# Optimization experiments

Hardware: AMD Instinct MI355X
Metric: run time of the kernel (lower is better)

Reference implementation:

```python
import jax, jax.numpy as jnp
import numpy as np
from jax import lax

C = 512   # n_feat == Cn == Cdim (forced by DA_conv/CA_layer consistency)
H, W = 16, 32  # reshape_codebooks(512)
K = 3     # kernel_size
RED = 8   # reduction


def _lrelu(x):
    return jax.nn.leaky_relu(x, 0.1)


def _conv1x1(x, w, b=None):
    # x: (B,C,H,W), w: (O,C) -- torch Conv2d(.,.,1) weight squeezed
    y = jnp.einsum('oc,bchw->bohw', w, x)
    if b is not None:
        y = y + b[None, :, None, None]
    return y


def _conv3x3(x, w, b):
    # x: (B,C,H,W), w: (O,C,3,3) OIHW, padding=k//2 == SAME for odd k
    y = lax.conv_general_dilated(x, w, (1, 1), 'SAME',
                                 dimension_numbers=('NCHW', 'OIHW', 'NCHW'))
    return y + b[None, :, None, None]


def _da_conv(c, deg, kw1, kw2, pw, pb, caw1, caw2):
    # per-channel dynamic kernels from degradation vectors: (Cn, K*K)
    kern = (_lrelu(deg @ kw1.T) @ kw2.T).reshape(C, 1, K, K)
    # depthwise conv, groups = b1*c1 = C (b1 == 1)
    out = lax.conv_general_dilated(c, kern, (1, 1), 'SAME',
                                   feature_group_count=C,
                                   dimension_numbers=('NCHW', 'OIHW', 'NCHW'))
    out = _lrelu(out)
    out = _conv1x1(out, pw, pb)
    # CA_layer: deg reshaped to (1, Cn, 16, 32), channel attention, deg * att
    dr = deg.reshape(1, C, H, W)
    att = jax.nn.sigmoid(_conv1x1(_lrelu(_conv1x1(dr, caw1)), caw2))
    return out + dr * att


def setup_inputs() -> dict:
    key = jax.random.key(0)
    ks = jax.random.split(key, 16)
    n = lambda i, shape, s=0.05: jax.random.normal(ks[i], shape, dtype=jnp.float32) * s
    return dict(
        c=jax.random.normal(ks[0], (1, C, H, W), dtype=jnp.float32),
        deg=jax.random.normal(ks[1], (C, C), dtype=jnp.float32) * 0.1,
        k1_w1=n(2, (C, C)), k1_w2=n(3, (K * K, C)),
        p1_w=n(4, (C, C)), p1_b=jnp.zeros((C,), jnp.float32),
        ca1_w1=n(5, (C // RED, C)), ca1_w2=n(6, (C, C // RED)),
        conv1_w=n(7, (C, C, K, K)), conv1_b=jnp.zeros((C,), jnp.float32),
        k2_w1=n(8, (C, C)), k2_w2=n(9, (K * K, C)),
        p2_w=n(10, (C, C)), p2_b=jnp.zeros((C,), jnp.float32),
        ca2_w1=n(11, (C // RED, C)), ca2_w2=n(12, (C, C // RED)),
        conv2_w=n(13, (C, C, K, K)), conv2_b=jnp.zeros((C,), jnp.float32),
    )


def reference(c, deg, k1_w1, k1_w2, p1_w, p1_b, ca1_w1, ca1_w2,
              conv1_w, conv1_b, k2_w1, k2_w2, p2_w, p2_b,
              ca2_w1, ca2_w2, conv2_w, conv2_b):
    out = _lrelu(_da_conv(c, deg, k1_w1, k1_w2, p1_w, p1_b, ca1_w1, ca1_w2))
    out = _lrelu(_conv3x3(out, conv1_w, conv1_b))
    out = _lrelu(_da_conv(out, deg, k2_w1, k2_w2, p2_w, p2_b, ca2_w1, ca2_w2))
    return _conv3x3(out, conv2_w, conv2_b) + c
```

## Files before the change

kernel.cpp:

```cpp
#include <hip/hip_runtime.h>
#include <hip/hip_bf16.h>

typedef __attribute__((ext_vector_type(8))) unsigned short ushort8;
typedef __attribute__((ext_vector_type(8))) __bf16 bf16x8;
typedef __attribute__((ext_vector_type(4))) float f32x4;
typedef __attribute__((ext_vector_type(4))) unsigned short ushort4v;

__device__ __forceinline__ float lrelu_f(float v){ return v > 0.f ? v : 0.1f*v; }

__device__ __forceinline__ unsigned short f2bf(float v){
  unsigned u = __float_as_uint(v);
  unsigned r = (u + 0x7fffu + ((u>>16)&1u)) >> 16;
  return (unsigned short)r;
}
__device__ __forceinline__ float bf2f(unsigned short u){
  return __uint_as_float(((unsigned)u)<<16);
}

__device__ __forceinline__ void gload16(const void* g, void* l){
  __builtin_amdgcn_global_load_lds(
    (const __attribute__((address_space(1))) unsigned int*)g,
    (__attribute__((address_space(3))) unsigned int*)l, 16, 0, 0);
}

__device__ __forceinline__ void packq(const float* __restrict__ s,
                                      unsigned short* __restrict__ d, int i){
  const float4 v = ((const float4*)s)[i];
  ushort4v o; o.x=f2bf(v.x); o.y=f2bf(v.y); o.z=f2bf(v.z); o.w=f2bf(v.w);
  *(ushort4v*)(d + (size_t)i*4) = o;
}

__global__ __launch_bounds__(256) void k_pack_all(
  const float* __restrict__ k1_w1, const float* __restrict__ k2_w1,
  const float* __restrict__ p1_w,  const float* __restrict__ p2_w,
  const float* __restrict__ ca1_w1,const float* __restrict__ ca1_w2,
  const float* __restrict__ ca2_w1,const float* __restrict__ ca2_w2,
  const float* __restrict__ deg,
  unsigned short* __restrict__ K1B, unsigned short* __restrict__ K2B,
  unsigned short* __restrict__ P1B, unsigned short* __restrict__ P2B,
  unsigned short* __restrict__ CA1A,unsigned short* __restrict__ CA1B,
  unsigned short* __restrict__ CA2A,unsigned short* __restrict__ CA2B,
  unsigned short* __restrict__ DEGB,unsigned short* __restrict__ DEGT){
  int i = blockIdx.x*256 + threadIdx.x;
  if (i < 65536){ packq(k1_w1, K1B, i); return; } i -= 65536;
  if (i < 65536){ packq(k2_w1, K2B, i); return; } i -= 65536;
  if (i < 65536){ packq(p1_w,  P1B, i); return; } i -= 65536;
  if (i < 65536){ packq(p2_w,  P2B, i); return; } i -= 65536;
  if (i < 8192){ packq(ca1_w1, CA1A, i); return; } i -= 8192;
  if (i < 8192){ packq(ca1_w2, CA1B, i); return; } i -= 8192;
  if (i < 8192){ packq(ca2_w1, CA2A, i); return; } i -= 8192;
  if (i < 8192){ packq(ca2_w2, CA2B, i); return; } i -= 8192;
  if (i < 65536){ packq(deg, DEGB, i); return; } i -= 65536;
  if (i < 65536){
    const int j = i*4; const int p = j>>9, c = j&511;
    ushort4v o;
    o.x = f2bf(deg[(size_t)(c+0)*512 + p]);
    o.y = f2bf(deg[(size_t)(c+1)*512 + p]);
    o.z = f2bf(deg[(size_t)(c+2)*512 + p]);
    o.w = f2bf(deg[(size_t)(c+3)*512 + p]);
    *(ushort4v*)(DEGT + (size_t)j) = o;
  }
}

__device__ __forceinline__ void gemm32(
    const unsigned short* __restrict__ A, const unsigned short* __restrict__ Bt,
    int m0, int n0, int K, int tid,
    unsigned short* lA, unsigned short* lB, f32x4& acc){
  const int wid = tid>>6, lane = tid&63;
  const int half = tid>>7, st_ = tid&127;
  const int srow = st_>>2, skb = st_&3;
  const unsigned short* gS = (half ? Bt + (size_t)(n0+srow)*K
                                   : A  + (size_t)(m0+srow)*K);
  unsigned short* lS = half ? lB : lA;
  const int soff0 = srow*64 + 8*(skb ^ (srow&7));
  const int soff1 = srow*64 + 8*((skb+4) ^ (srow&7));

  const int wr = (wid>>1)*16, wc = (wid&1)*16;
  const int l15 = lane&15, lkb = lane>>4;
  int aoff[2], boff[2];
  #pragma unroll
  for (int h=0;h<2;h++){
    const int Ra = wr + l15;
    aoff[h] = Ra*64 + 8*((lkb+4*h) ^ (Ra&7));
    const int Rb = wc + l15;
    boff[h] = Rb*64 + 8*((lkb+4*h) ^ (Rb&7));
  }

  const int nst = K>>6;
  ushort8 r0 = *(const ushort8*)(gS + skb*8);
  ushort8 r1 = *(const ushort8*)(gS + (skb+4)*8);
  *(ushort8*)(lS + soff0) = r0;
  *(ushort8*)(lS + soff1) = r1;
  if (nst > 1){
    r0 = *(const ushort8*)(gS + 64 + skb*8);
    r1 = *(const ushort8*)(gS + 64 + (skb+4)*8);
  }
  __syncthreads();
  for (int st=0; st<nst; ++st){
    const int cur = (st&1)*2048;
    bf16x8 af[2], bf[2];
    #pragma unroll
    for (int h=0;h<2;h++){
      af[h] = *(const bf16x8*)(lA + cur + aoff[h]);
      bf[h] = *(const bf16x8*)(lB + cur + boff[h]);
    }
    if (st+1 < nst){
      const int nxt = ((st+1)&1)*2048;
      *(ushort8*)(lS + nxt + soff0) = r0;
      *(ushort8*)(lS + nxt + soff1) = r1;
      if (st+2 < nst){
        r0 = *(const ushort8*)(gS + (size_t)(st+2)*64 + skb*8);
        r1 = *(const ushort8*)(gS + (size_t)(st+2)*64 + (skb+4)*8);
      }
    }
    #pragma unroll
    for (int h=0;h<2;h++)
      acc = __builtin_amdgcn_mfma_f32_16x16x32_bf16(af[h], bf[h], acc, 0,0,0);
    __syncthreads();
  }
}

__global__ __launch_bounds__(256) void k_mgemm_pre(
    const unsigned short* __restrict__ DEGB, const unsigned short* __restrict__ DEGT,
    const unsigned short* __restrict__ K1B,  const unsigned short* __restrict__ K2B,
    const unsigned short* __restrict__ CA1A, const unsigned short* __restrict__ CA2A,
    const float* __restrict__ conv1_w, const float* __restrict__ conv2_w,
    float* __restrict__ TMP1, float* __restrict__ TMP2,
    unsigned short* __restrict__ HID1, unsigned short* __restrict__ HID2,
    unsigned short* __restrict__ WB1, unsigned short* __restrict__ WB2){
  const int z = blockIdx.z;
  if (z >= 2 && blockIdx.y >= 2){
    const float* src      = (z==2) ? conv1_w : conv2_w;
    unsigned short* dst   = (z==2) ? WB1 : WB2;
    const int base = (((blockIdx.y-2)*16 + blockIdx.x)*256) + threadIdx.x;
    for (int i = base; i < 589824; i += 57344){
      const int o_ = i/1152; const int r4 = (i - o_*1152)*4;
      const int t = r4>>9; const int ci = r4&511;
      const float* s = src + (size_t)o_*4608;
      ushort4v o;
      o.x = f2bf(s[(ci+0)*9 + t]); o.y = f2bf(s[(ci+1)*9 + t]);
      o.z = f2bf(s[(ci+2)*9 + t]); o.w = f2bf(s[(ci+3)*9 + t]);
      *(ushort4v*)(dst + (size_t)o_*4608 + r4) = o;
    }
    return;
  }
  const unsigned short* A  = (z < 2) ? DEGB : DEGT;
  const unsigned short* Bt = (z==0) ? K1B : (z==1) ? K2B : (z==2) ? CA1A : CA2A;
  __shared__ unsigned short lA[4096], lB[4096];
  const int tid = threadIdx.x;
  const int m0 = blockIdx.x*32, n0 = blockIdx.y*32;
  f32x4 acc = {};
  gemm32(A, Bt, m0, n0, 512, tid, lA, lB, acc);

  const int wid = tid>>6, lane = tid&63;
  const int wr = (wid>>1)*16, wc = (wid&1)*16;
  const int l15 = lane&15, lkb = lane>>4;
  #pragma unroll
  for (int r=0;r<4;r++){
    const int row = m0 + wr + lkb*4 + r;
    const int col = n0 + wc + l15;
    const float v = lrelu_f(acc[r]);
    if (z==0)      TMP1[(size_t)row*512 + col] = v;
    else if (z==1) TMP2[(size_t)row*512 + col] = v;
    else if (z==2) HID1[(size_t)row*64 + col] = f2bf(v);
    else           HID2[(size_t)row*64 + col] = f2bf(v);
  }
}

__device__ __forceinline__ void gemm64(
    const unsigned short* __restrict__ A, const unsigned short* __restrict__ Bt,
    int m0, int n0, int K, int tid,
    unsigned short* lA, unsigned short* lB, f32x4 acc[2][2]){
  const int wid = tid>>6, lane = tid&63;
  const int srow = tid>>2, skb = tid&3;
  const unsigned short* gA = A  + (size_t)(m0+srow)*K + skb*8;
  const unsigned short* gB = Bt + (size_t)(n0+srow)*K + skb*8;
  const int soff = srow*32 + 8*(skb ^ (srow&3));
  const int wr = (wid>>1)*32, wc = (wid&1)*32;
  const int l15 = lane&15, lkb = lane>>4;
  int aoff[2], boff[2];
  #pragma unroll
  for (int s=0;s<2;s++){
    const int Ra = wr + s*16 + l15;
    aoff[s] = Ra*32 + 8*(lkb ^ (Ra&3));
    const int Rb = wc + s*16 + l15;
    boff[s] = Rb*32 + 8*(lkb ^ (Rb&3));
  }
  const int nst = K>>5;
  ushort8 ra = *(const ushort8*)gA;
  ushort8 rb = *(const ushort8*)gB;
  *(ushort8*)(lA + soff) = ra;
  *(ushort8*)(lB + soff) = rb;
  if (nst > 1){ ra = *(const ushort8*)(gA+32); rb = *(const ushort8*)(gB+32); }
  __syncthreads();
  for (int st=0; st<nst; ++st){
    const int cur = (st&1)*2048;
    bf16x8 af[2], bfr[2];
    #pragma unroll
    for (int s=0;s<2;s++){
      af[s]  = *(const bf16x8*)(lA + cur + aoff[s]);
      bfr[s] = *(const bf16x8*)(lB + cur + boff[s]);
    }
    if (st+1 < nst){
      const int nxt = ((st+1)&1)*2048;
      *(ushort8*)(lA + nxt + soff) = ra;
      *(ushort8*)(lB + nxt + soff) = rb;
      if (st+2 < nst){
        ra = *(const ushort8*)(gA + (size_t)(st+2)*32);
        rb = *(const ushort8*)(gB + (size_t)(st+2)*32);
      }
    }
    #pragma unroll
    for (int mi=0;mi<2;mi++)
      #pragma unroll
      for (int ni=0;ni<2;ni++)
        acc[mi][ni] = __builtin_amdgcn_mfma_f32_16x16x32_bf16(af[mi], bfr[ni], acc[mi][ni], 0,0,0);
    __syncthreads();
  }
}

__global__ __launch_bounds__(256) void k_kern_att(
    const float* __restrict__ TMP1, const float* __restrict__ TMP2,
    const float* __restrict__ kw2a, const float* __restrict__ kw2b,
    const unsigned short* __restrict__ CA1B, const unsigned short* __restrict__ CA2B,
    const unsigned short* __restrict__ HID1, const unsigned short* __restrict__ HID2,
    float* __restrict__ kern0, float* __restrict__ kern1,
    float* __restrict__ ATT1, float* __restrict__ ATT2,
    unsigned short* __restrict__ XTP){
  const int z = blockIdx.z;
  const int tid = threadIdx.x;
  if (z < 2){
    const float* tmp  = z ? TMP2 : TMP1;
    const float* kw2  = z ? kw2b : kw2a;
    float* kern       = z ? kern1 : kern0;
    const int i = blockIdx.x*4 + (tid>>6);
    const int lane = tid&63;
    float acc[9];
    #pragma unroll
    for (int q=0;q<9;q++) acc[q]=0.f;
    for (int j=lane; j<512; j+=64){
      const float t = tmp[i*512 + j];
      #pragma unroll
      for (int q=0;q<9;q++) acc[q] += t*kw2[q*512 + j];
    }
    #pragma unroll
    for (int q=0;q<9;q++){
      float v = acc[q];
      #pragma unroll
      for (int off=32; off>0; off>>=1) v += __shfl_down(v, off);
      if (lane==0) kern[i*9+q] = v;
    }
  } else {
    if (blockIdx.x >= 64){
      if (z==2){
        const int idx = (blockIdx.x-64)*256 + tid;
        if (idx < 12800){
          const int si = idx>>7, wi = idx&127;
          int slot;
          if (si < 34) slot = si;
          else if (si < 68) slot = 578 + (si-34);
          else if (si < 84) slot = (si-67)*34;
          else slot = (si-83)*34 + 33;
          ushort4v zz = {};
          *(ushort4v*)(XTP + (size_t)slot*512 + wi*4) = zz;
        }
      }
      return;
    }
    const unsigned short* A  = (z==2) ? CA1B : CA2B;
    const unsigned short* Bt = (z==2) ? HID1 : HID2;
    float* ATT               = (z==2) ? ATT1 : ATT2;
    __shared__ unsigned short lA[4096], lB[4096];
    const int m0 = (blockIdx.x>>3)*64, n0 = (blockIdx.x&7)*64;
    f32x4 acc[2][2] = {};
    gemm64(A, Bt, m0, n0, 64, tid, lA, lB, acc);
    const int wid = tid>>6, lane = tid&63;
    const int wr = (wid>>1)*32, wc = (wid&1)*32;
    const int l15 = lane&15, lkb = lane>>4;
    #pragma unroll
    for (int mi=0;mi<2;mi++)
      #pragma unroll
      for (int ni=0;ni<2;ni++){
        const int row = m0 + wr + mi*16 + lkb*4;
        const int col = n0 + wc + ni*16 + l15;
        #pragma unroll
        for (int r=0;r<4;r++)
          ATT[(size_t)(row+r)*512 + col] = 1.f/(1.f + expf(-acc[mi][ni][r]));
      }
  }
}

__global__ __launch_bounds__(512) void k_dwconv(const float* __restrict__ x,
    const float* __restrict__ kern, unsigned short* __restrict__ yt){
  const int c = blockIdx.x;
  const int p = threadIdx.x;
  const int iy = p>>5, ix = p&31;
  __shared__ float plane[18*34];
  for (int i=p;i<18*34;i+=512) plane[i]=0.f;
  __syncthreads();
  plane[(iy+1)*34 + ix+1] = x[c*512 + p];
  __syncthreads();
  const float* kp = kern + c*9;
  float s = 0.f;
  #pragma unroll
  for (int dy=0;dy<3;dy++)
    #pragma unroll
    for (int dx=0;dx<3;dx++)
      s += plane[(iy+dy)*34 + ix+dx]*kp[dy*3+dx];
  yt[(size_t)p*512 + c] = f2bf(lrelu_f(s));
}

__global__ __launch_bounds__(512) void k_dwconv_red(const unsigned short* __restrict__ part,
    const float* __restrict__ bias, const float* __restrict__ kern,
    unsigned short* __restrict__ yt, int nchunks){
  const int c = blockIdx.x;
  const int p = threadIdx.x;
  const int iy = p>>5, ix = p&31;
  __shared__ float plane[18*34];
  for (int i=p;i<18*34;i+=512) plane[i]=0.f;
  __syncthreads();
  if (p < 128){
    const float b = bias[c];
    float4 a4 = {b,b,b,b};
    for (int s=0;s<nchunks;s++){
      const ushort4v v = ((const ushort4v*)(part + (size_t)s*262144 + c*512))[p];
      a4.x += bf2f(v.x); a4.y += bf2f(v.y); a4.z += bf2f(v.z); a4.w += bf2f(v.w);
    }
    a4.x = lrelu_f(a4.x); a4.y = lrelu_f(a4.y);
    a4.z = lrelu_f(a4.z); a4.w = lrelu_f(a4.w);
    const int px0 = p*4;
    float* dst = &plane[((px0>>5)+1)*34 + (px0&31)+1];
    dst[0]=a4.x; dst[1]=a4.y; dst[2]=a4.z; dst[3]=a4.w;
  }
  __syncthreads();
  const float* kp = kern + c*9;
  float s = 0.f;
  #pragma unroll
  for (int dy=0;dy<3;dy++)
    #pragma unroll
    for (int dx=0;dx<3;dx++)
      s += plane[(iy+dy)*34 + ix+dx]*kp[dy*3+dx];
  yt[(size_t)p*512 + c] = f2bf(lrelu_f(s));
}

__global__ __launch_bounds__(256) void k_pw(
    const unsigned short* __restrict__ A, const unsigned short* __restrict__ Bt,
    const float* __restrict__ bias,
    const float* __restrict__ E1, const float* __restrict__ E2,
    unsigned short* __restrict__ XTP){
  __shared__ unsigned short lA[4096], lB[4096];
  __shared__ float tile[32][33];
  const int tid = threadIdx.x;
  const int wid = tid>>6, lane = tid&63;
  const int M0 = blockIdx.x*32, N0 = blockIdx.y*32;

  f32x4 acc = {};
  gemm32(A, Bt, M0, N0, 512, tid, lA, lB, acc);

  const int wr = (wid>>1)*16, wc = (wid&1)*16;
  const int l15 = lane&15, lkb = lane>>4;
  #pragma unroll
  for (int r=0;r<4;r++){
    const int rl = wr + lkb*4 + r;
    const int cl = wc + l15;
    const int rr = M0 + rl, col = N0 + cl;
    float v = acc[r] + bias[rr] + E1[(size_t)rr*512+col]*E2[(size_t)rr*512+col];
    tile[rl][cl] = lrelu_f(v);
  }
  __syncthreads();
  const int pr = tid>>3, q = tid&7;
  const int p = N0 + pr;
  const int slot = ((p>>5)+1)*34 + (p&31) + 1;
  ushort4v o;
  o.x = f2bf(tile[q*4+0][pr]); o.y = f2bf(tile[q*4+1][pr]);
  o.z = f2bf(tile[q*4+2][pr]); o.w = f2bf(tile[q*4+3][pr]);
  *(ushort4v*)(XTP + (size_t)slot*512 + M0 + q*4) = o;
}

template<int KCH>
__global__ __launch_bounds__(256) void k_mfma_conv(
    const unsigned short* __restrict__ WB,
    const unsigned short* __restrict__ XTP,
    unsigned short* __restrict__ part){
  __shared__ __attribute__((aligned(16))) unsigned short lA[2][4096];
  __shared__ __attribute__((aligned(16))) unsigned short lB[2][8192];
  const int tid = threadIdx.x;
  const int wid = tid>>6, lane = tid&63;
  const int m0 = blockIdx.x*64, n0 = blockIdx.y*128;
  const int k0 = blockIdx.z*KCH;

  const int wrow = wid*8 + (lane>>3);
  const int clin = lane&7;
  const unsigned short* asrc[2];
  #pragma unroll
  for (int j=0;j<2;j++){
    const int r = j*32 + wrow;
    asrc[j] = WB + (size_t)(m0+r)*4608 + k0 + (clin ^ (r&7))*8;
  }
  int bpy[4], bpx[4], bchk[4];
  #pragma unroll
  for (int j=0;j<4;j++){
    const int r = j*32 + wrow;
    const int pp = n0 + r;
    bpy[j] = pp>>5; bpx[j] = pp&31;
    bchk[j] = (clin ^ (r&7))*8;
  }

  const int wr = (wid>>1)*32, wc = (wid&1)*64;
  const int l15 = lane&15, lkb = lane>>4;
  int aoff[2][2], boff[4][2];
  #pragma unroll
  for (int s=0;s<2;s++){
    const int Ra = wr + s*16 + l15;
    #pragma unroll
    for (int h=0;h<2;h++) aoff[s][h] = Ra*64 + 8*((lkb+4*h) ^ (Ra&7));
  }
  #pragma unroll
  for (int u=0;u<4;u++){
    const int Rb = wc + u*16 + l15;
    #pragma unroll
    for (int h=0;h<2;h++) boff[u][h] = Rb*64 + 8*((lkb+4*h) ^ (Rb&7));
  }

  auto stage = [&](int buf, int st){
    #pragma unroll
    for (int j=0;j<2;j++)
      gload16(asrc[j] + st*64, &lA[buf][j*2048 + wid*512]);
    const int k = k0 + st*64;
    const int t = k>>9;
    const int dy = t/3, dx = t - dy*3;
    const int kc = k & 511;
    #pragma unroll
    for (int j=0;j<4;j++){
      const int slot = (bpy[j]+dy)*34 + bpx[j]+dx;
      gload16(XTP + (size_t)slot*512 + kc + bchk[j],
              &lB[buf][j*2048 + wid*512]);
    }
  };

  constexpr int NST = KCH/64;
  f32x4 acc[2][4] = {};
  stage(0, 0);
  __syncthreads();
  #pragma unroll
  for (int st=0; st<NST; ++st){
    const int cur = st&1;
    if (st+1 < NST) stage(cur^1, st+1);
    bf16x8 af[2][2], bfr[4][2];
    #pragma unroll
    for (int s=0;s<2;s++)
      #pragma unroll
      for (int h=0;h<2;h++) af[s][h] = *(const bf16x8*)(&lA[cur][aoff[s][h]]);
    #pragma unroll
    for (int u=0;u<4;u++)
      #pragma unroll
      for (int h=0;h<2;h++) bfr[u][h] = *(const bf16x8*)(&lB[cur][boff[u][h]]);
    #pragma unroll
    for (int h=0;h<2;h++)
      #pragma unroll
      for (int s=0;s<2;s++)
        #pragma unroll
        for (int u=0;u<4;u++)
          acc[s][u] = __builtin_amdgcn_mfma_f32_16x16x32_bf16(af[s][h], bfr[u][h], acc[s][u], 0,0,0);
    __syncthreads();
  }

  unsigned short* pbase = part + (size_t)blockIdx.z*262144;
  #pragma unroll
  for (int s=0;s<2;s++)
    #pragma unroll
    for (int u=0;u<4;u++){
      const int row = m0 + wr + s*16 + lkb*4;
      const int col = n0 + wc + u*16 + l15;
      #pragma unroll
      for (int r=0;r<4;r++)
        pbase[(size_t)(row+r)*512 + col] = f2bf(acc[s][u][r]);
    }
}

__global__ __launch_bounds__(256) void k_reduce_final(const unsigned short* __restrict__ part,
    const float* __restrict__ bias, const float* __restrict__ res,
    float* __restrict__ y, int nchunks){
  const int i = blockIdx.x*256 + threadIdx.x;
  const int o = i>>7;
  const float b = bias[o];
  float4 a4 = {b,b,b,b};
  for (int s=0;s<nchunks;s++){
    const ushort4v v = ((const ushort4v*)part)[(size_t)s*65536 + i];
    a4.x += bf2f(v.x); a4.y += bf2f(v.y); a4.z += bf2f(v.z); a4.w += bf2f(v.w);
  }
  const float4 rv = ((const float4*)res)[i];
  a4.x += rv.x; a4.y += rv.y; a4.z += rv.z; a4.w += rv.w;
  ((float4*)y)[i] = a4;
}

extern "C" void kernel_launch(void* const* d_in, const int* in_sizes, int n_in,
                              void* d_out, int out_size, void* d_ws, size_t ws_size,
                              hipStream_t stream) {
  (void)in_sizes; (void)n_in; (void)out_size; (void)ws_size;
  const float* xin    = (const float*)d_in[0];
  const float* deg    = (const float*)d_in[1];
  const float* k1_w1  = (const float*)d_in[2];
  const float* k1_w2  = (const float*)d_in[3];
  const float* p1_w   = (const float*)d_in[4];
  const float* p1_b   = (const float*)d_in[5];
  const float* ca1_w1 = (const float*)d_in[6];
  const float* ca1_w2 = (const float*)d_in[7];
  const float* conv1_w= (const float*)d_in[8];
  const float* conv1_b= (const float*)d_in[9];
  const float* k2_w1  = (const float*)d_in[10];
  const float* k2_w2  = (const float*)d_in[11];
  const float* p2_w   = (const float*)d_in[12];
  const float* p2_b   = (const float*)d_in[13];
  const float* ca2_w1 = (const float*)d_in[14];
  const float* ca2_w2 = (const float*)d_in[15];
  const float* conv2_w= (const float*)d_in[16];
  const float* conv2_b= (const float*)d_in[17];
  float* out = (float*)d_out;

  const int NS = 18;

  float* ws = (float*)d_ws;
  unsigned short* PART = (unsigned short*)ws;
  ws += (size_t)NS*131072;
  float* TMP1 = (float*)PART;
  float* TMP2 = TMP1 + 262144;
  unsigned short* HID1 = (unsigned short*)(TMP2 + 262144);
  unsigned short* HID2 = HID1 + 32768;
  float* KERN1 = ws;  ws += 4608;
  float* KERN2 = ws;  ws += 4608;
  float* ATT1  = ws;  ws += 262144;
  float* ATT2  = ws;  ws += 262144;
  unsigned short* DEGB = (unsigned short*)ws; ws += 131072;
  unsigned short* DEGT = (unsigned short*)ws; ws += 131072;
  unsigned short* K1B  = (unsigned short*)ws; ws += 131072;
  unsigned short* K2B  = (unsigned short*)ws; ws += 131072;
  unsigned short* XTP  = K1B;
  unsigned short* P1B  = (unsigned short*)ws; ws += 131072;
  unsigned short* P2B  = (unsigned short*)ws; ws += 131072;
  unsigned short* CA1A = (unsigned short*)ws; ws += 16384;
  unsigned short* CA1B = (unsigned short*)ws; ws += 16384;
  unsigned short* CA2A = (unsigned short*)ws; ws += 16384;
  unsigned short* CA2B = (unsigned short*)ws; ws += 16384;
  unsigned short* DWLT = (unsigned short*)ws; ws += 131072;
  unsigned short* WB1  = (unsigned short*)ws; ws += 1179648;
  unsigned short* WB2  = (unsigned short*)ws; ws += 1179648;

  k_pack_all<<<1664,256,0,stream>>>(k1_w1,k2_w1,p1_w,p2_w,
      ca1_w1,ca1_w2,ca2_w1,ca2_w2, deg,
      K1B,K2B,P1B,P2B, CA1A,CA1B,CA2A,CA2B, DEGB,DEGT);

  k_mgemm_pre<<<dim3(16,16,4),256,0,stream>>>(DEGB,DEGT, K1B,K2B, CA1A,CA2A,
      conv1_w, conv2_w, TMP1,TMP2, HID1,HID2, WB1,WB2);
  k_kern_att<<<dim3(128,1,4),256,0,stream>>>(TMP1,TMP2, k1_w2,k2_w2,
      CA1B,CA2B, HID1,HID2, KERN1,KERN2, ATT1,ATT2, XTP);

  k_dwconv<<<512,512,0,stream>>>(xin, KERN1, DWLT);
  k_pw<<<dim3(16,16),256,0,stream>>>(P1B, DWLT, p1_b, deg, ATT1, XTP);
  k_mfma_conv<256><<<dim3(8,4,18),256,0,stream>>>(WB1, XTP, PART);
  k_dwconv_red<<<512,512,0,stream>>>(PART, conv1_b, KERN2, DWLT, NS);
  k_pw<<<dim3(16,16),256,0,stream>>>(P2B, DWLT, p2_b, deg, ATT2, XTP);
  k_mfma_conv<256><<<dim3(8,4,18),256,0,stream>>>(WB2, XTP, PART);
  k_reduce_final<<<256,256,0,stream>>>(PART, conv2_b, xin, out, NS);
}
```

Measured before the change: 81.70 us.

## Fuse kernel-weight projection into GEMM epilogue and merge attention with dwconv

The second small projection (lrelu(deg@kw1^T)@kw2^T) moves into the epilogue of the first GEMM. Each block reduces its 32-column slice to per-row 9-tap partials, and those partials are later summed across 16 column chunks by the depthwise conv kernels. This removes the fp32 TMP intermediate round trip and the separate k_kern_att reduction launch. The CA attention GEMM, the XTP halo zeroing and the first depthwise conv are merged into one launch, cutting the launch count by one. In exchange there are extra shuffle reductions in the GEMM epilogue and redundant 16-way partial sums in every dwconv block.

```diff
diff --git a/kernel.cpp b/kernel.cpp
--- a/kernel.cpp
+++ b/kernel.cpp
@@ -125,14 +125,16 @@
     const unsigned short* __restrict__ K1B,  const unsigned short* __restrict__ K2B,
     const unsigned short* __restrict__ CA1A, const unsigned short* __restrict__ CA2A,
     const float* __restrict__ conv1_w, const float* __restrict__ conv2_w,
-    float* __restrict__ TMP1, float* __restrict__ TMP2,
+    const float* __restrict__ kw2a, const float* __restrict__ kw2b,
+    float* __restrict__ KP1, float* __restrict__ KP2,
     unsigned short* __restrict__ HID1, unsigned short* __restrict__ HID2,
     unsigned short* __restrict__ WB1, unsigned short* __restrict__ WB2){
   const int z = blockIdx.z;
+  const int tid = threadIdx.x;
   if (z >= 2 && blockIdx.y >= 2){
     const float* src      = (z==2) ? conv1_w : conv2_w;
     unsigned short* dst   = (z==2) ? WB1 : WB2;
-    const int base = (((blockIdx.y-2)*16 + blockIdx.x)*256) + threadIdx.x;
+    const int base = (((blockIdx.y-2)*16 + blockIdx.x)*256) + tid;
     for (int i = base; i < 589824; i += 57344){
       const int o_ = i/1152; const int r4 = (i - o_*1152)*4;
       const int t = r4>>9; const int ci = r4&511;
@@ -144,26 +146,55 @@
     }
     return;
   }
-  const unsigned short* A  = (z < 2) ? DEGB : DEGT;
-  const unsigned short* Bt = (z==0) ? K1B : (z==1) ? K2B : (z==2) ? CA1A : CA2A;
   __shared__ unsigned short lA[4096], lB[4096];
-  const int tid = threadIdx.x;
-  const int m0 = blockIdx.x*32, n0 = blockIdx.y*32;
-  f32x4 acc = {};
-  gemm32(A, Bt, m0, n0, 512, tid, lA, lB, acc);
-
+  __shared__ float kp[2][32][9];
   const int wid = tid>>6, lane = tid&63;
-  const int wr = (wid>>1)*16, wc = (wid&1)*16;
   const int l15 = lane&15, lkb = lane>>4;
-  #pragma unroll
-  for (int r=0;r<4;r++){
-    const int row = m0 + wr + lkb*4 + r;
-    const int col = n0 + wc + l15;
-    const float v = lrelu_f(acc[r]);
-    if (z==0)      TMP1[(size_t)row*512 + col] = v;
-    else if (z==1) TMP2[(size_t)row*512 + col] = v;
-    else if (z==2) HID1[(size_t)row*64 + col] = f2bf(v);
-    else           HID2[(size_t)row*64 + col] = f2bf(v);
+
+  if (z < 2){
+    const int it = blockIdx.x, jc = blockIdx.y;
+    const unsigned short* Bt = z ? K2B : K1B;
+    const float* kw2 = z ? kw2b : kw2a;
+    float* KP        = z ? KP2 : KP1;
+    const int m0 = it*32, n0 = jc*32;
+    f32x4 acc = {};
+    gemm32(DEGB, Bt, m0, n0, 512, tid, lA, lB, acc);
+
+    const int wr = (wid>>1)*16, wc2 = wid&1;
+    const int col = n0 + wc2*16 + l15;
+    float w[9];
+    #pragma unroll
+    for (int t=0;t<9;t++) w[t] = kw2[t*512 + col];
+    #pragma unroll
+    for (int r=0;r<4;r++){
+      const float v = lrelu_f(acc[r]);
+      const int row = wr + lkb*4 + r;
+      #pragma unroll
+      for (int t=0;t<9;t++){
+        float q = v*w[t];
+        q += __shfl_xor(q,1); q += __shfl_xor(q,2);
+        q += __shfl_xor(q,4); q += __shfl_xor(q,8);
+        if (l15==0) kp[wc2][row][t] = q;
+      }
+    }
+    __syncthreads();
+    for (int i = tid; i < 288; i += 256){
+      const int row = i/9, t = i - row*9;
+      KP[((size_t)jc*512 + m0 + row)*9 + t] = kp[0][row][t] + kp[1][row][t];
+    }
+  } else {
+    const unsigned short* caw = (z==2) ? CA1A : CA2A;
+    unsigned short* HID = (z==2) ? HID1 : HID2;
+    const int m0 = blockIdx.x*32, n0 = blockIdx.y*32;
+    f32x4 acc = {};
+    gemm32(DEGT, caw, m0, n0, 512, tid, lA, lB, acc);
+    const int wr = (wid>>1)*16, wc = (wid&1)*16;
+    #pragma unroll
+    for (int r=0;r<4;r++){
+      const int row = m0 + wr + lkb*4 + r;
+      const int col = n0 + wc + l15;
+      HID[(size_t)row*64 + col] = f2bf(lrelu_f(acc[r]));
+    }
   }
 }
 
@@ -219,59 +250,23 @@
   }
 }
 
-__global__ __launch_bounds__(256) void k_kern_att(
-    const float* __restrict__ TMP1, const float* __restrict__ TMP2,
-    const float* __restrict__ kw2a, const float* __restrict__ kw2b,
+__global__ __launch_bounds__(256) void k_att_dw(
     const unsigned short* __restrict__ CA1B, const unsigned short* __restrict__ CA2B,
     const unsigned short* __restrict__ HID1, const unsigned short* __restrict__ HID2,
-    float* __restrict__ kern0, float* __restrict__ kern1,
     float* __restrict__ ATT1, float* __restrict__ ATT2,
-    unsigned short* __restrict__ XTP){
-  const int z = blockIdx.z;
+    const float* __restrict__ xin, const float* __restrict__ KP1,
+    unsigned short* __restrict__ DWLT, unsigned short* __restrict__ XTP){
+  __shared__ __align__(16) unsigned char smem[16640];
   const int tid = threadIdx.x;
-  if (z < 2){
-    const float* tmp  = z ? TMP2 : TMP1;
-    const float* kw2  = z ? kw2b : kw2a;
-    float* kern       = z ? kern1 : kern0;
-    const int i = blockIdx.x*4 + (tid>>6);
-    const int lane = tid&63;
-    float acc[9];
-    #pragma unroll
-    for (int q=0;q<9;q++) acc[q]=0.f;
-    for (int j=lane; j<512; j+=64){
-      const float t = tmp[i*512 + j];
-      #pragma unroll
-      for (int q=0;q<9;q++) acc[q] += t*kw2[q*512 + j];
-    }
-    #pragma unroll
-    for (int q=0;q<9;q++){
-      float v = acc[q];
-      #pragma unroll
-      for (int off=32; off>0; off>>=1) v += __shfl_down(v, off);
-      if (lane==0) kern[i*9+q] = v;
-    }
-  } else {
-    if (blockIdx.x >= 64){
-      if (z==2){
-        const int idx = (blockIdx.x-64)*256 + tid;
-        if (idx < 12800){
-          const int si = idx>>7, wi = idx&127;
-          int slot;
-          if (si < 34) slot = si;
-          else if (si < 68) slot = 578 + (si-34);
-          else if (si < 84) slot = (si-67)*34;
-          else slot = (si-83)*34 + 33;
-          ushort4v zz = {};
-          *(ushort4v*)(XTP + (size_t)slot*512 + wi*4) = zz;
-        }
-      }
-      return;
-    }
-    const unsigned short* A  = (z==2) ? CA1B : CA2B;
-    const unsigned short* Bt = (z==2) ? HID1 : HID2;
-    float* ATT               = (z==2) ? ATT1 : ATT2;
-    __shared__ unsigned short lA[4096], lB[4096];
-    const int m0 = (blockIdx.x>>3)*64, n0 = (blockIdx.x&7)*64;
+  int bid = blockIdx.x;
+  if (bid < 128){
+    unsigned short* lA = (unsigned short*)smem;
+    unsigned short* lB = lA + 4096;
+    const int b = bid>>6, t6 = bid&63;
+    const unsigned short* A   = b ? CA2B : CA1B;
+    const unsigned short* Bt  = b ? HID2 : HID1;
+    float* ATT                = b ? ATT2 : ATT1;
+    const int m0 = (t6>>3)*64, n0 = (t6&7)*64;
     f32x4 acc[2][2] = {};
     gemm64(A, Bt, m0, n0, 64, tid, lA, lB, acc);
     const int wid = tid>>6, lane = tid&63;
@@ -287,37 +282,67 @@
         for (int r=0;r<4;r++)
           ATT[(size_t)(row+r)*512 + col] = 1.f/(1.f + expf(-acc[mi][ni][r]));
       }
-  }
-}
-
-__global__ __launch_bounds__(512) void k_dwconv(const float* __restrict__ x,
-    const float* __restrict__ kern, unsigned short* __restrict__ yt){
-  const int c = blockIdx.x;
-  const int p = threadIdx.x;
-  const int iy = p>>5, ix = p&31;
-  __shared__ float plane[18*34];
-  for (int i=p;i<18*34;i+=512) plane[i]=0.f;
-  __syncthreads();
-  plane[(iy+1)*34 + ix+1] = x[c*512 + p];
-  __syncthreads();
-  const float* kp = kern + c*9;
-  float s = 0.f;
-  #pragma unroll
-  for (int dy=0;dy<3;dy++)
-    #pragma unroll
-    for (int dx=0;dx<3;dx++)
-      s += plane[(iy+dy)*34 + ix+dx]*kp[dy*3+dx];
-  yt[(size_t)p*512 + c] = f2bf(lrelu_f(s));
+  } else {
+    bid -= 128;
+    const int c = bid;
+    {
+      const int idx = bid*256 + tid;
+      if (idx < 12800){
+        const int si = idx>>7, wi = idx&127;
+        int slot;
+        if (si < 34) slot = si;
+        else if (si < 68) slot = 578 + (si-34);
+        else if (si < 84) slot = (si-67)*34;
+        else slot = (si-83)*34 + 33;
+        ushort4v zz = {};
+        *(ushort4v*)(XTP + (size_t)slot*512 + wi*4) = zz;
+      }
+    }
+    float* plane = (float*)smem;
+    float* ks = plane + 612;
+    for (int i=tid;i<612;i+=256) plane[i]=0.f;
+    if (tid<9){
+      float s=0.f;
+      #pragma unroll
+      for (int jc=0;jc<16;jc++) s += KP1[((size_t)jc*512 + c)*9 + tid];
+      ks[tid]=s;
+    }
+    #pragma unroll
+    for (int q=0;q<2;q++){
+      const int px = tid + q*256;
+      plane[((px>>5)+1)*34 + (px&31)+1] = xin[(size_t)c*512 + px];
+    }
+    __syncthreads();
+    #pragma unroll
+    for (int q=0;q<2;q++){
+      const int px = tid + q*256;
+      const int iy = px>>5, ix = px&31;
+      float s = 0.f;
+      #pragma unroll
+      for (int dy=0;dy<3;dy++)
+        #pragma unroll
+        for (int dx=0;dx<3;dx++)
+          s += plane[(iy+dy)*34 + ix+dx]*ks[dy*3+dx];
+      DWLT[(size_t)px*512 + c] = f2bf(lrelu_f(s));
+    }
+  }
 }
 
 __global__ __launch_bounds__(512) void k_dwconv_red(const unsigned short* __restrict__ part,
-    const float* __restrict__ bias, const float* __restrict__ kern,
+    const float* __restrict__ bias, const float* __restrict__ KP,
     unsigned short* __restrict__ yt, int nchunks){
   const int c = blockIdx.x;
   const int p = threadIdx.x;
   const int iy = p>>5, ix = p&31;
   __shared__ float plane[18*34];
+  __shared__ float ks[9];
   for (int i=p;i<18*34;i+=512) plane[i]=0.f;
+  if (p < 9){
+    float s = 0.f;
+    #pragma unroll
+    for (int jc=0;jc<16;jc++) s += KP[((size_t)jc*512 + c)*9 + p];
+    ks[p] = s;
+  }
   __syncthreads();
   if (p < 128){
     const float b = bias[c];
@@ -333,13 +358,12 @@
     dst[0]=a4.x; dst[1]=a4.y; dst[2]=a4.z; dst[3]=a4.w;
   }
   __syncthreads();
-  const float* kp = kern + c*9;
   float s = 0.f;
   #pragma unroll
   for (int dy=0;dy<3;dy++)
     #pragma unroll
     for (int dx=0;dx<3;dx++)
-      s += plane[(iy+dy)*34 + ix+dx]*kp[dy*3+dx];
+      s += plane[(iy+dy)*34 + ix+dx]*ks[dy*3+dx];
   yt[(size_t)p*512 + c] = f2bf(lrelu_f(s));
 }
 
@@ -523,14 +547,12 @@
   float* ws = (float*)d_ws;
   unsigned short* PART = (unsigned short*)ws;
   ws += (size_t)NS*131072;
-  float* TMP1 = (float*)PART;
-  float* TMP2 = TMP1 + 262144;
-  unsigned short* HID1 = (unsigned short*)(TMP2 + 262144);
+  unsigned short* HID1 = PART;
   unsigned short* HID2 = HID1 + 32768;
-  float* KERN1 = ws;  ws += 4608;
-  float* KERN2 = ws;  ws += 4608;
-  float* ATT1  = ws;  ws += 262144;
-  float* ATT2  = ws;  ws += 262144;
+  float* KP1  = ws;  ws += 73728;
+  float* KP2  = ws;  ws += 73728;
+  float* ATT1 = ws;  ws += 262144;
+  float* ATT2 = ws;  ws += 262144;
   unsigned short* DEGB = (unsigned short*)ws; ws += 131072;
   unsigned short* DEGT = (unsigned short*)ws; ws += 131072;
   unsigned short* K1B  = (unsigned short*)ws; ws += 131072;
@@ -551,14 +573,14 @@
       K1B,K2B,P1B,P2B, CA1A,CA1B,CA2A,CA2B, DEGB,DEGT);
 
   k_mgemm_pre<<<dim3(16,16,4),256,0,stream>>>(DEGB,DEGT, K1B,K2B, CA1A,CA2A,
-      conv1_w, conv2_w, TMP1,TMP2, HID1,HID2, WB1,WB2);
-  k_kern_att<<<dim3(128,1,4),256,0,stream>>>(TMP1,TMP2, k1_w2,k2_w2,
-      CA1B,CA2B, HID1,HID2, KERN1,KERN2, ATT1,ATT2, XTP);
-
-  k_dwconv<<<512,512,0,stream>>>(xin, KERN1, DWLT);
+      conv1_w, conv2_w, k1_w2, k2_w2, KP1,KP2, HID1,HID2, WB1,WB2);
+
+  k_att_dw<<<640,256,0,stream>>>(CA1B,CA2B, HID1,HID2, ATT1,ATT2,
+      xin, KP1, DWLT, XTP);
+
   k_pw<<<dim3(16,16),256,0,stream>>>(P1B, DWLT, p1_b, deg, ATT1, XTP);
   k_mfma_conv<256><<<dim3(8,4,18),256,0,stream>>>(WB1, XTP, PART);
-  k_dwconv_red<<<512,512,0,stream>>>(PART, conv1_b, KERN2, DWLT, NS);
+  k_dwconv_red<<<512,512,0,stream>>>(PART, conv1_b, KP2, DWLT, NS);
   k_pw<<<dim3(16,16),256,0,stream>>>(P2B, DWLT, p2_b, deg, ATT2, XTP);
   k_mfma_conv<256><<<dim3(8,4,18),256,0,stream>>>(WB2, XTP, PART);
   k_reduce_final<<<256,256,0,stream>>>(PART, conv2_b, xin, out, NS);
```

After: 75.94 us, median of 2. 7.1% less time.
